# Kernel tuning notes

Hardware: AMD Instinct MI355X
Metric: run time of the kernel (lower is better)

Reference implementation:

```python
import jax, jax.numpy as jnp
import numpy as np

N, E, G = 8192, 65536, 16          # nodes, edges, graphs
EMBED, HID, L = 512, 1024, 3       # embed_dim, hidden_dim, hidden_layers
NG, RBF_R = 50, 12.0               # num_gaussians, rbf_radius
AVG_LEN = 60.0
IN_DIM = 3 * EMBED


def _mlp_params(key, in_dim, hid, out_dim, n_layers):
    ks = jax.random.split(key, 6)
    s_in = 1.0 / np.sqrt(in_dim)
    s_h = 1.0 / np.sqrt(hid)
    return dict(
        in_w=jax.random.normal(ks[0], (in_dim, hid), jnp.float32) * s_in,
        in_b=jnp.zeros((hid,), jnp.float32),
        hid_w=jax.random.normal(ks[1], (n_layers, hid, hid), jnp.float32) * s_h,
        hid_b=jnp.zeros((n_layers, hid), jnp.float32),
        out_w=jax.random.normal(ks[2], (hid, out_dim), jnp.float32) * s_h,
        out_b=jnp.zeros((out_dim,), jnp.float32),
    )


def setup_inputs() -> dict:
    key = jax.random.key(0)
    k = jax.random.split(key, 8)
    x = jax.random.normal(k[0], (N, EMBED), jnp.float32)
    edge_index = jax.random.randint(k[1], (2, E), 0, N, dtype=jnp.int32)
    batch = jnp.sort(jax.random.randint(k[2], (N,), 0, G, dtype=jnp.int32))
    dist = jax.random.uniform(k[3], (E,), jnp.float32) * RBF_R
    v = jax.random.normal(k[4], (E, 3), jnp.float32)
    vec_hat = v / jnp.linalg.norm(v, axis=-1, keepdims=True)
    rbf_w = jax.random.normal(k[5], (NG, EMBED), jnp.float32) * (1.0 / np.sqrt(NG))
    rbf_b = jnp.zeros((EMBED,), jnp.float32)
    e = _mlp_params(k[6], IN_DIM, HID, 1, L)
    f = _mlp_params(k[7], IN_DIM, HID, 1, L)
    return dict(
        x=x, edge_index=edge_index, batch=batch, dist=dist, vec_hat=vec_hat,
        rbf_w=rbf_w, rbf_b=rbf_b,
        e_in_w=e['in_w'], e_in_b=e['in_b'], e_hid_w=e['hid_w'], e_hid_b=e['hid_b'], e_out_w=e['out_w'], e_out_b=e['out_b'],
        f_in_w=f['in_w'], f_in_b=f['in_b'], f_hid_w=f['hid_w'], f_hid_b=f['hid_b'], f_out_w=f['out_w'], f_out_b=f['out_b'],
    )


def _res_mlp(h_in, in_w, in_b, hid_w, hid_b, out_w, out_b):
    h = jax.nn.silu(h_in @ in_w + in_b)           # [E, HID]
    for i in range(L):                             # residual hidden blocks
        h = h + jax.nn.silu(h @ hid_w[i] + hid_b[i])
    return h @ out_w + out_b                       # [E, 1]


def _rbf(dist, rbf_w, rbf_b):
    offsets = jnp.linspace(0.0, RBF_R, NG)
    coeff = -0.5 / (offsets[1] - offsets[0]) ** 2
    g = jnp.exp(coeff * (dist[:, None] - offsets) ** 2)  # [E, NG]
    return g @ rbf_w + rbf_b                              # [E, EMBED]


def reference(x, edge_index, batch, dist, vec_hat,
              rbf_w, rbf_b,
              e_in_w, e_in_b, e_hid_w, e_hid_b, e_out_w, e_out_b,
              f_in_w, f_in_b, f_hid_w, f_hid_b, f_out_w, f_out_b):
    src, dst = edge_index[0], edge_index[1]
    rbf = _rbf(dist, rbf_w, rbf_b)                                 # [E, EMBED]
    inputs = jnp.concatenate([x[src], x[dst], rbf], axis=-1)       # [E, 3*EMBED]
    energy_pairs = _res_mlp(inputs, e_in_w, e_in_b, e_hid_w, e_hid_b, e_out_w, e_out_b)  # [E,1]
    force_pairs = _res_mlp(inputs, f_in_w, f_in_b, f_hid_w, f_hid_b, f_out_w, f_out_b) * vec_hat  # [E,3]
    energy = jax.ops.segment_sum(energy_pairs, batch[src], num_segments=G) / (AVG_LEN ** 2)  # [G,1]
    forces = jax.ops.segment_sum(force_pairs, src, num_segments=N) / AVG_LEN                 # [N,3]
    return energy, forces
```

## Files before the change

kernel.cpp:

```cpp
#include <hip/hip_runtime.h>
#include <math.h>

#define NUM_E 65536
#define NUM_N 8192
#define NUM_G 16
#define RBFR 12.0f

typedef unsigned short u16;
typedef _Float16 f16x8 __attribute__((ext_vector_type(8)));
typedef _Float16 f16x4 __attribute__((ext_vector_type(4)));
typedef float f32x4 __attribute__((ext_vector_type(4)));

#define TILE_F16 8192
#define L1SZ   1114112
#define HSZ    1048576
#define MSTRIDE 4259840

#define FU1  139264
#define FUHL 131072
#define FUPM (FU1 + 3 * FUHL)

#define GLD16(gp, lp) __builtin_amdgcn_global_load_lds( \
    (const __attribute__((address_space(1))) void*)(gp), \
    (__attribute__((address_space(3))) void*)(lp), 16, 0, 0)

#define VMW10() asm volatile("s_waitcnt vmcnt(10)" ::: "memory")
#define VMW8()  asm volatile("s_waitcnt vmcnt(8)" ::: "memory")
#define VMW4()  asm volatile("s_waitcnt vmcnt(4)" ::: "memory")
#define VMW0()  asm volatile("s_waitcnt vmcnt(0)" ::: "memory")
#define BARX()  __builtin_amdgcn_s_barrier()

__global__ void wrbf_kernel(const float* __restrict__ rbf_w, const float* __restrict__ rbf_b,
                            const float* __restrict__ e_in_w, const float* __restrict__ e_in_b,
                            const float* __restrict__ f_in_w, const float* __restrict__ f_in_b,
                            float* __restrict__ wrbf_e, float* __restrict__ b1_e,
                            float* __restrict__ wrbf_f, float* __restrict__ b1_f) {
  int blk = blockIdx.x;
  int mlp = blk / 204;
  int rr = blk % 204;
  int row = rr >> 2;
  int ns = rr & 3;
  const float* in_w = mlp ? f_in_w : e_in_w;
  const float* in_b = mlp ? f_in_b : e_in_b;
  float* wrbf = mlp ? wrbf_f : wrbf_e;
  float* b1   = mlp ? b1_f : b1_e;
  __shared__ float vec[512];
  __shared__ float4 red[256];
  int tid = threadIdx.x;
  vec[tid]       = (row < 50) ? rbf_w[row * 512 + tid]       : rbf_b[tid];
  vec[tid + 256] = (row < 50) ? rbf_w[row * 512 + tid + 256] : rbf_b[tid + 256];
  __syncthreads();
  int q = tid >> 6, l = tid & 63;
  int n0 = ns * 256 + l * 4;
  float a0 = 0.f, a1 = 0.f, a2 = 0.f, a3 = 0.f;
#pragma unroll 4
  for (int c = q * 128; c < q * 128 + 128; ++c) {
    float4 wv = *(const float4*)&in_w[(size_t)(1024 + c) * 1024 + n0];
    float gv = vec[c];
    a0 += gv * wv.x; a1 += gv * wv.y; a2 += gv * wv.z; a3 += gv * wv.w;
  }
  red[tid] = float4{a0, a1, a2, a3};
  __syncthreads();
  if (q == 0) {
    float4 s0 = red[l], s1 = red[l + 64], s2 = red[l + 128], s3 = red[l + 192];
    float4 o = {s0.x + s1.x + s2.x + s3.x, s0.y + s1.y + s2.y + s3.y,
                s0.z + s1.z + s2.z + s3.z, s0.w + s1.w + s2.w + s3.w};
    if (row < 50) {
      *(float4*)&wrbf[row * 1024 + n0] = o;
    } else {
      o.x += in_b[n0]; o.y += in_b[n0 + 1]; o.z += in_b[n0 + 2]; o.w += in_b[n0 + 3];
      *(float4*)&b1[n0] = o;
    }
  }
}

__global__ void prep_kernel(const float* __restrict__ x, const float* __restrict__ dist,
                            u16* __restrict__ xh, u16* __restrict__ grbf) {
  int bid = blockIdx.x, tid = threadIdx.x;
  if (bid < 4096) {
    int i = bid * 256 + tid;
    float4 v = ((const float4*)x)[i];
    f16x4 h = {(_Float16)v.x, (_Float16)v.y, (_Float16)v.z, (_Float16)v.w};
    *(f16x4*)(xh + (size_t)i * 4) = h;
  } else {
    int u = (bid - 4096) * 256 + tid;
    int e = u >> 3, q = u & 7;
    const float delta = RBFR / 49.f;
    const float coeff = -0.5f / (delta * delta);
    float d = dist[e];
    f16x8 h;
#pragma unroll
    for (int j = 0; j < 8; ++j) {
      int gi = q * 8 + j;
      float dd = d - (float)gi * delta;
      float gg = (gi < 50) ? __expf(coeff * dd * dd) : 0.f;
      h[j] = (_Float16)gg;
    }
    *(f16x8*)(grbf + (size_t)u * 8) = h;
  }
}

__global__ void pack_gemm(const float* __restrict__ e_in_w, const float* __restrict__ e_hid_w,
                          const float* __restrict__ f_in_w, const float* __restrict__ f_hid_w,
                          const float* __restrict__ wrbf_e, const float* __restrict__ wrbf_f,
                          u16* __restrict__ wp) {
  __shared__ __align__(16) u16 tile[TILE_F16];
  int bid = blockIdx.x;
  int mlpi = (bid >= 520) ? 1 : 0;
  int t = bid - mlpi * 520;
  const float* in_w  = mlpi ? f_in_w : e_in_w;
  const float* hid_w = mlpi ? f_hid_w : e_hid_w;
  const float* wrbf  = mlpi ? wrbf_f : wrbf_e;
  int tid = threadIdx.x;
  int bnp, nhp, k0, lay = 0, is_l1;
  if (t < 136) {
    int grp = t / 17; int kt = t % 17;
    bnp = grp >> 1; nhp = grp & 1; k0 = kt * 64; is_l1 = 1;
  } else {
    int th = t - 136; lay = th >> 7; int t2 = th & 127;
    bnp = t2 >> 5; nhp = (t2 >> 4) & 1; k0 = (t2 & 15) * 64; is_l1 = 0;
  }
#pragma unroll
  for (int it = 0; it < 8; ++it) {
    int flat = it * 1024 + tid * 4;
    int k = flat >> 7;
    int nl4 = flat & 127;
    int n0 = bnp * 256 + ((nl4 >> 5) << 6) + nhp * 32 + (nl4 & 31);
    int kg = k0 + k;
    float4 v;
    if (is_l1) {
      if (kg < 1024)      v = *(const float4*)&in_w[(size_t)kg * 1024 + n0];
      else if (kg < 1074) v = *(const float4*)&wrbf[(size_t)(kg - 1024) * 1024 + n0];
      else                v = float4{0.f, 0.f, 0.f, 0.f};
    } else {
      v = *(const float4*)&hid_w[(size_t)((lay << 10) + kg) * 1024 + n0];
    }
#pragma unroll
    for (int c = 0; c < 4; ++c) {
      int nl = nl4 + c;
      int pos = nl * 64 + ((((k >> 3) ^ (nl & 7)) << 3) | (k & 7));
      _Float16 hf = (_Float16)(((const float*)&v)[c]);
      tile[pos] = __builtin_bit_cast(u16, hf);
    }
  }
  __syncthreads();
  u16* dst = wp + (size_t)mlpi * MSTRIDE + (size_t)t * TILE_F16;
#pragma unroll
  for (int i = 0; i < 4; ++i) {
    int off = (i * 256 + tid) * 8;
    *(f16x8*)(dst + off) = *(const f16x8*)(tile + off);
  }
}


#define STA(b, ah, kt) do { \
  _Pragma("unroll") for (int _j = 0; _j < 2; ++_j) { \
    int _ck = wv * 2 + _j; \
    int _loc = _ck * 8 + (lane >> 3); \
    int _row = ((_loc >> 6) << 7) + (ah) * 64 + (_loc & 63); \
    int _sw = ((lane & 7) ^ (_loc & 7)) << 3; \
    const u16* _gp; \
    if (MODE == 1) { \
      if ((kt) < 16) { \
        int _nd = ((kt) < 8) ? s_src[_row] : s_dst[_row]; \
        _gp = hin + ((size_t)_nd * 512 + ((kt) & 7) * 64 + _sw); \
      } else { \
        _gp = grbf + ((size_t)(eg0 + _row) * 64 + _sw); \
      } \
    } else { \
      _gp = hin + ((size_t)(rowb + _row) * 1024 + (kt) * 64 + _sw); \
    } \
    GLD16(_gp, (char*)&sm[b][ah][0] + _ck * 1024); \
  } \
} while (0)

#define STB(b, bh, kt) do { \
  const u16* _wt = wl + ((size_t)((bn * 2 + (bh)) * NKT + (kt))) * TILE_F16; \
  _Pragma("unroll") for (int _j = 0; _j < 2; ++_j) { \
    int _ck = wv * 2 + _j; \
    GLD16(_wt + _ck * 512 + lane * 8, (char*)&sm[b][2 + (bh)][0] + _ck * 1024); \
  } \
} while (0)

#define RDA(b, mh) do { \
  _Pragma("unroll") for (int _ks = 0; _ks < 2; ++_ks) { \
    int _kk = _ks * 4 + (lane >> 4); \
    _Pragma("unroll") for (int _m = 0; _m < 4; ++_m) { \
      int _r = wm * 64 + _m * 16 + (lane & 15); \
      af[_m][_ks] = *(const f16x8*)&sm[b][mh][_r * 64 + ((_kk ^ (_r & 7)) << 3)]; \
    } \
  } \
} while (0)

#define RDB(b, nh) do { \
  _Pragma("unroll") for (int _ks = 0; _ks < 2; ++_ks) { \
    int _kk = _ks * 4 + (lane >> 4); \
    _Pragma("unroll") for (int _n = 0; _n < 2; ++_n) { \
      int _c = wn * 32 + _n * 16 + (lane & 15); \
      bf[nh][_n][_ks] = *(const f16x8*)&sm[b][2 + (nh)][_c * 64 + ((_kk ^ (_c & 7)) << 3)]; \
    } \
  } \
} while (0)

#define PHM(mh, nh) do { \
  __builtin_amdgcn_s_setprio(1); \
  _Pragma("unroll") for (int _ks = 0; _ks < 2; ++_ks) \
    _Pragma("unroll") for (int _m = 0; _m < 4; ++_m) \
      _Pragma("unroll") for (int _n = 0; _n < 2; ++_n) \
        acc[(mh) * 4 + _m][(nh) * 2 + _n] = __builtin_amdgcn_mfma_f32_16x16x32_f16( \
            bf[nh][_n][_ks], af[_m][_ks], acc[(mh) * 4 + _m][(nh) * 2 + _n], 0, 0, 0); \
  __builtin_amdgcn_s_setprio(0); \
} while (0)

template<int NKT, int MODE>
__global__ __launch_bounds__(512, 2) void gemm8k(
    const u16* __restrict__ hinE, const u16* __restrict__ hinF,
    const u16* __restrict__ grbf, const int* __restrict__ eidx,
    const int* __restrict__ batch, const float* __restrict__ vhat,
    const u16* __restrict__ wp, size_t woff,
    const float* __restrict__ biasE, const float* __restrict__ biasF,
    u16* __restrict__ houtE, u16* __restrict__ houtF,
    const float* __restrict__ owE, const float* __restrict__ owF,
    const float* __restrict__ obE, const float* __restrict__ obF,
    float* __restrict__ out, int mstart) {
  __shared__ __align__(16) u16 sm[2][4][8192];
  __shared__ int s_src[256];
  __shared__ int s_dst[256];
  __shared__ float sred[256];
  __shared__ float sbins[16];
  const int tid = threadIdx.x;
  const int lane = tid & 63;
  const int wv = tid >> 6;
  const int wm = wv >> 2, wn = wv & 3;

  int mlp, mt, bn;
  {
    int xcd = blockIdx.x & 7;
    int r = blockIdx.x >> 3;
    if (MODE == 1) {
      int bnq = r & 7;
      mlp = bnq >> 2; bn = bnq & 3;
      mt = (r >> 3) * 8 + xcd;
    } else {
      bn = r & 3; mlp = (r >> 2) & 1;
      mt = (r >> 3) * 8 + xcd;
    }
  }
  const u16* hin = (MODE == 1) ? hinE : (mlp ? hinF : hinE);
  const u16* wl = wp + (size_t)mlp * MSTRIDE + woff;
  const float* bias = mlp ? biasF : biasE;
  u16* hout = mlp ? houtF : houtE;
  const int rowb = mt * 256;
  const int n0 = bn * 256;
  const int eg0 = mstart + rowb;

  if (MODE == 1) {
    if (tid < 256) s_src[tid] = eidx[eg0 + tid];
    else s_dst[tid - 256] = eidx[NUM_E + eg0 + tid - 256];
    __syncthreads();
  }

  f32x4 acc[8][4];
#pragma unroll
  for (int m = 0; m < 8; ++m)
#pragma unroll
    for (int n = 0; n < 4; ++n)
#pragma unroll
      for (int i = 0; i < 4; ++i) acc[m][n][i] = 0.f;

  f16x8 af[4][2], bf[2][2][2];

  STA(0, 0, 0); STB(0, 0, 0); STB(0, 1, 0); STA(0, 1, 0);
  VMW4(); BARX();

  for (int t = 0; t < NKT - 1; ++t) {
    const int b = t & 1, nb = b ^ 1;
    STA(nb, 0, t + 1); STB(nb, 0, t + 1); STB(nb, 1, t + 1); STA(nb, 1, t + 1);
    RDA(b, 0); RDB(b, 0);
    VMW10(); BARX();
    PHM(0, 0);
    RDB(b, 1);
    VMW8(); BARX();
    PHM(0, 1);
    RDA(b, 1);
    PHM(1, 0);
    VMW4(); BARX();
    PHM(1, 1);
  }
  {
    const int tb = (NKT - 1) & 1;
    RDA(tb, 0); RDB(tb, 0);
    PHM(0, 0);
    VMW0(); BARX();
    RDB(tb, 1); PHM(0, 1);
    RDA(tb, 1); PHM(1, 0); PHM(1, 1);
  }

  if (MODE != 2) {
#pragma unroll
    for (int mi = 0; mi < 8; ++mi) {
#pragma unroll
      for (int ni = 0; ni < 4; ++ni) {
        int grow = rowb + wm * 128 + mi * 16 + (lane & 15);
        int gn = n0 + wn * 64 + ni * 16 + ((lane >> 4) << 2);
        float4 bi = *(const float4*)&bias[gn];
        f16x4 o;
        if (MODE == 1) {
#pragma unroll
          for (int i = 0; i < 4; ++i) {
            float pre = acc[mi][ni][i] + ((const float*)&bi)[i];
            o[i] = (_Float16)(pre / (1.f + __expf(-pre)));
          }
        } else {
          f16x4 hp = *(const f16x4*)&hin[(size_t)grow * 1024 + gn];
#pragma unroll
          for (int i = 0; i < 4; ++i) {
            float pre = acc[mi][ni][i] + ((const float*)&bi)[i];
            o[i] = (_Float16)(pre / (1.f + __expf(-pre)) + (float)hp[i]);
          }
        }
        *(f16x4*)&hout[(size_t)grow * 1024 + gn] = o;
      }
    }
  } else {
    if (tid < 256) sred[tid] = 0.f;
    if (tid < 16) sbins[tid] = 0.f;
    __syncthreads();
    const float* ow = mlp ? owF : owE;
    float p[8];
#pragma unroll
    for (int mi = 0; mi < 8; ++mi) p[mi] = 0.f;
#pragma unroll
    for (int mi = 0; mi < 8; ++mi) {
#pragma unroll
      for (int ni = 0; ni < 4; ++ni) {
        int grow = rowb + wm * 128 + mi * 16 + (lane & 15);
        int gn = n0 + wn * 64 + ni * 16 + ((lane >> 4) << 2);
        float4 bi = *(const float4*)&bias[gn];
        float4 wv4 = *(const float4*)&ow[gn];
        f16x4 hp = *(const f16x4*)&hin[(size_t)grow * 1024 + gn];
#pragma unroll
        for (int i = 0; i < 4; ++i) {
          float pre = acc[mi][ni][i] + ((const float*)&bi)[i];
          float val = pre / (1.f + __expf(-pre)) + (float)hp[i];
          p[mi] += val * ((const float*)&wv4)[i];
        }
      }
    }
#pragma unroll
    for (int mi = 0; mi < 8; ++mi) {
      p[mi] += __shfl_down(p[mi], 32, 64);
      p[mi] += __shfl_down(p[mi], 16, 64);
    }
    if ((lane >> 4) == 0) {
#pragma unroll
      for (int mi = 0; mi < 8; ++mi)
        atomicAdd(&sred[wm * 128 + mi * 16 + (lane & 15)], p[mi]);
    }
    __syncthreads();
    if (tid < 256) {
      float s = sred[tid];
      int eg = eg0 + tid;
      int si = eidx[eg];
      if (mlp == 0) {
        float pv = s + ((bn == 0) ? obE[0] : 0.f);
        atomicAdd(&sbins[batch[si]], pv);
      } else {
        float pv = (s + ((bn == 0) ? obF[0] : 0.f)) * (1.f / 60.f);
        atomicAdd(&out[16 + si * 3 + 0], pv * vhat[(size_t)eg * 3 + 0]);
        atomicAdd(&out[16 + si * 3 + 1], pv * vhat[(size_t)eg * 3 + 1]);
        atomicAdd(&out[16 + si * 3 + 2], pv * vhat[(size_t)eg * 3 + 2]);
      }
    }
    __syncthreads();
    if (mlp == 0 && tid < 16) atomicAdd(&out[tid], sbins[tid] * (1.f / 3600.f));
  }
}

#define FSWZ(row, col) ((((row) * 1088) + (col)) ^ (((row) & 7) << 3))

__global__ void packF_kernel(const float* __restrict__ e_in_w, const float* __restrict__ e_hid_w,
                             const float* __restrict__ f_in_w, const float* __restrict__ f_hid_w,
                             const float* __restrict__ wrbf_e, const float* __restrict__ wrbf_f,
                             u16* __restrict__ wp) {
  int u = blockIdx.x * 256 + threadIdx.x;
  if (u >= 2 * FUPM) return;
  int m = (u >= FUPM) ? 1 : 0;
  int v = u - m * FUPM;
  const float* in_w  = m ? f_in_w : e_in_w;
  const float* hid_w = m ? f_hid_w : e_hid_w;
  const float* wrbf  = m ? wrbf_f : wrbf_e;
  int l = v & 63;
  int kb = (l >> 4) << 3;
  f16x8 vals;
  if (v < FU1) {
    int kt = v >> 12;
    int ntg = (v >> 6) & 63;
    int n = ntg * 16 + (l & 15);
    int k0 = kt * 32 + kb;
#pragma unroll
    for (int jj = 0; jj < 8; ++jj) {
      int k = k0 + jj;
      float f = (k < 1024) ? in_w[(size_t)k * 1024 + n]
              : ((k < 1074) ? wrbf[(k - 1024) * 1024 + n] : 0.f);
      vals[jj] = (_Float16)f;
    }
  } else {
    int vh = v - FU1;
    int lay = vh >> 17;
    int kt = (vh >> 12) & 31;
    int ntg = (vh >> 6) & 63;
    int n = ntg * 16 + (l & 15);
    int k0 = kt * 32 + kb;
#pragma unroll
    for (int jj = 0; jj < 8; ++jj)
      vals[jj] = (_Float16)hid_w[(size_t)((lay << 10) + k0 + jj) * 1024 + n];
  }
  *(f16x8*)(wp + (size_t)u * 8) = vals;
}

#define F_LOADB(buf, kt) do { \
  const u16* _wr = wl + ((size_t)((kt) * 64 + wave * 8) * 64 + lane) * 8; \
  _Pragma("unroll") \
  for (int _nt = 0; _nt < 8; ++_nt) buf[_nt] = *(const f16x8*)(_wr + (size_t)_nt * 512); \
} while (0)
#define F_LOADA(buf, kt) do { \
  const int _kb = (kt) * 32 + ((lane >> 4) << 3); \
  _Pragma("unroll") \
  for (int _r = 0; _r < 4; ++_r) buf[_r] = *(const f16x8*)&Alds[FSWZ(_r * 16 + (lane & 15), _kb)]; \
} while (0)
#define F_MFMAS(abuf, bbuf) do { \
  _Pragma("unroll") \
  for (int _nt = 0; _nt < 8; ++_nt) \
    _Pragma("unroll") \
    for (int _r = 0; _r < 4; ++_r) \
      acc[_r][_nt] = __builtin_amdgcn_mfma_f32_16x16x32_f16(abuf[_r], bbuf[_nt], acc[_r][_nt], 0, 0, 0); \
} while (0)

__global__ __launch_bounds__(512, 2) void fusedF_kernel(
    const float* __restrict__ x, const int* __restrict__ eidx,
    const int* __restrict__ batch, const float* __restrict__ dist,
    const float* __restrict__ vhat,
    const u16* __restrict__ wp,
    const float* __restrict__ b1_e, const float* __restrict__ b1_f,
    const float* __restrict__ e_hid_b, const float* __restrict__ f_hid_b,
    const float* __restrict__ e_out_w, const float* __restrict__ e_out_b,
    const float* __restrict__ f_out_w, const float* __restrict__ f_out_b,
    float* __restrict__ out) {
  __shared__ __align__(16) u16 Alds[64 * 1088];
  __shared__ float sow[1024];
  __shared__ float sbins[16];
  __shared__ int s_src[64];
  __shared__ int s_dst[64];
  __shared__ float s_dist[64];
  const int tid = threadIdx.x;
  const int lane = tid & 63;
  const int wave = tid >> 6;
  const int e0 = blockIdx.x * 64;
  if (tid < 16) sbins[tid] = 0.f;
  if (tid < 64) s_src[tid] = eidx[e0 + tid];
  if (tid >= 64 && tid < 128) s_dst[tid - 64] = eidx[NUM_E + e0 + tid - 64];
  if (tid >= 128 && tid < 192) s_dist[tid - 128] = dist[e0 + tid - 128];
  __syncthreads();
  const float delta = RBFR / 49.f;
  const float coeff = -0.5f / (delta * delta);
  for (int mlp = 0; mlp < 2; ++mlp) {
    for (int i = tid; i < 16384; i += 512) {
      int e = i >> 8;
      int part = (i >> 7) & 1;
      int q = i & 127;
      int nrow = part ? s_dst[e] : s_src[e];
      float4 v = ((const float4*)x)[(size_t)nrow * 128 + q];
      int col = part * 512 + q * 4;
      f16x4 hv = {(_Float16)v.x, (_Float16)v.y, (_Float16)v.z, (_Float16)v.w};
      *(f16x4*)&Alds[FSWZ(e, col)] = hv;
    }
    for (int i = tid; i < 4096; i += 512) {
      int e = i >> 6;
      int gi = i & 63;
      float d = s_dist[e] - (float)gi * delta;
      float g2 = (gi < 50) ? __expf(coeff * d * d) : 0.f;
      _Float16 hg = (_Float16)g2;
      Alds[FSWZ(e, 1024 + gi)] = __builtin_bit_cast(u16, hg);
    }
    __syncthreads();
    const u16* wp1 = wp + (size_t)mlp * FUPM * 8;
    const u16* wph = wp1 + (size_t)FU1 * 8;
    const float* b1 = mlp ? b1_f : b1_e;
    const float* hb = mlp ? f_hid_b : e_hid_b;
    for (int layer = 0; layer < 4; ++layer) {
      const int nkt = (layer == 0) ? 34 : 32;
      const u16* wl = (layer == 0) ? wp1 : (wph + (size_t)(layer - 1) * FUHL * 8);
      const float* bias = (layer == 0) ? b1 : (hb + (layer - 1) * 1024);
      f32x4 acc[4][8];
#pragma unroll
      for (int r = 0; r < 4; ++r)
#pragma unroll
        for (int nt = 0; nt < 8; ++nt)
#pragma unroll
          for (int i = 0; i < 4; ++i) acc[r][nt][i] = 0.f;
      f16x8 a0[4], a1[4], b0[8], b1r[8];
      F_LOADA(a0, 0); F_LOADB(b0, 0);
      F_LOADA(a1, 1); F_LOADB(b1r, 1);
      for (int kt = 0; kt < nkt; kt += 2) {
        F_MFMAS(a0, b0);
        if (kt + 2 < nkt) { F_LOADA(a0, kt + 2); F_LOADB(b0, kt + 2); }
        F_MFMAS(a1, b1r);
        if (kt + 3 < nkt) { F_LOADA(a1, kt + 3); F_LOADB(b1r, kt + 3); }
      }
      __syncthreads();
      float bia[8];
#pragma unroll
      for (int nt = 0; nt < 8; ++nt) bia[nt] = bias[wave * 128 + nt * 16 + (lane & 15)];
#pragma unroll
      for (int r = 0; r < 4; ++r) {
#pragma unroll
        for (int nt = 0; nt < 8; ++nt) {
#pragma unroll
          for (int i = 0; i < 4; ++i) {
            int row = r * 16 + ((lane >> 4) << 2) + i;
            int col = wave * 128 + nt * 16 + (lane & 15);
            float pre = acc[r][nt][i] + bia[nt];
            float val = pre / (1.f + __expf(-pre));
            int idx = FSWZ(row, col);
            if (layer > 0) {
              _Float16 oldh = __builtin_bit_cast(_Float16, Alds[idx]);
              val += (float)oldh;
            }
            _Float16 nh = (_Float16)val;
            Alds[idx] = __builtin_bit_cast(u16, nh);
          }
        }
      }
      __syncthreads();
    }
    const float* ow = mlp ? f_out_w : e_out_w;
    for (int i = tid; i < 1024; i += 512) sow[i] = ow[i];
    __syncthreads();
    {
      int e = tid >> 3;
      int part = tid & 7;
      float s = 0.f;
#pragma unroll
      for (int cc = 0; cc < 16; ++cc) {
        int col = part * 128 + cc * 8;
        f16x8 hv = *(const f16x8*)&Alds[FSWZ(e, col)];
#pragma unroll
        for (int q = 0; q < 8; ++q) s += (float)hv[q] * sow[col + q];
      }
      s += __shfl_down(s, 4, 8);
      s += __shfl_down(s, 2, 8);
      s += __shfl_down(s, 1, 8);
      if (part == 0) {
        if (mlp == 0) {
          float pp = s + e_out_b[0];
          int gg = batch[s_src[e]];
          atomicAdd(&sbins[gg], pp);
        } else {
          float pp = (s + f_out_b[0]) * (1.f / 60.f);
          int si = s_src[e];
          atomicAdd(&out[16 + si * 3 + 0], pp * vhat[(size_t)(e0 + e) * 3 + 0]);
          atomicAdd(&out[16 + si * 3 + 1], pp * vhat[(size_t)(e0 + e) * 3 + 1]);
          atomicAdd(&out[16 + si * 3 + 2], pp * vhat[(size_t)(e0 + e) * 3 + 2]);
        }
      }
    }
    __syncthreads();
  }
  if (tid < 16) atomicAdd(&out[tid], sbins[tid] * (1.f / 3600.f));
}

extern "C" void kernel_launch(void* const* d_in, const int* in_sizes, int n_in,
                              void* d_out, int out_size, void* d_ws, size_t ws_size,
                              hipStream_t stream) {
  (void)in_sizes; (void)n_in;
  const float* x      = (const float*)d_in[0];
  const int*   eidx   = (const int*)d_in[1];
  const int*   batch  = (const int*)d_in[2];
  const float* dist   = (const float*)d_in[3];
  const float* vhat   = (const float*)d_in[4];
  const float* rbf_w  = (const float*)d_in[5];
  const float* rbf_b  = (const float*)d_in[6];
  const float* e_in_w = (const float*)d_in[7];
  const float* e_in_b = (const float*)d_in[8];
  const float* e_hid_w = (const float*)d_in[9];
  const float* e_hid_b = (const float*)d_in[10];
  const float* e_out_w = (const float*)d_in[11];
  const float* e_out_b = (const float*)d_in[12];
  const float* f_in_w = (const float*)d_in[13];
  const float* f_in_b = (const float*)d_in[14];
  const float* f_hid_w = (const float*)d_in[15];
  const float* f_hid_b = (const float*)d_in[16];
  const float* f_out_w = (const float*)d_in[17];
  const float* f_out_b = (const float*)d_in[18];

  const size_t WP_BYTES = 17039360;
  u16* wp       = (u16*)d_ws;
  float* wrbf_e = (float*)((char*)d_ws + WP_BYTES);
  float* wrbf_f = wrbf_e + 50 * 1024;
  float* b1_e   = wrbf_f + 50 * 1024;
  float* b1_f   = b1_e + 1024;
  const size_t BASE = WP_BYTES + 409600 + 8192;
  u16* xh   = (u16*)((char*)d_ws + BASE);
  u16* grbf = (u16*)((char*)d_ws + BASE + 8388608);
  const size_t FIXED = BASE + 16777216;

  int nch = 0;
  for (int c = 1; c <= 8; c <<= 1) {
    size_t need = FIXED + 4 * (size_t)(NUM_E / c) * 1024 * sizeof(u16);
    if (need <= ws_size) { nch = c; break; }
  }

  hipMemsetAsync(d_out, 0, (size_t)out_size * sizeof(float), stream);
  wrbf_kernel<<<408, 256, 0, stream>>>(rbf_w, rbf_b, e_in_w, e_in_b, f_in_w, f_in_b,
                                       wrbf_e, b1_e, wrbf_f, b1_f);

  if (nch == 0) {
    packF_kernel<<<(2 * FUPM + 255) / 256, 256, 0, stream>>>(
        e_in_w, e_hid_w, f_in_w, f_hid_w, wrbf_e, wrbf_f, wp);
    fusedF_kernel<<<NUM_E / 64, 512, 0, stream>>>(x, eidx, batch, dist, vhat, wp,
                                                  b1_e, b1_f, e_hid_b, f_hid_b,
                                                  e_out_w, e_out_b, f_out_w, f_out_b,
                                                  (float*)d_out);
    return;
  }

  pack_gemm<<<1040, 256, 0, stream>>>(
      e_in_w, e_hid_w, f_in_w, f_hid_w, wrbf_e, wrbf_f, wp);
  prep_kernel<<<6144, 256, 0, stream>>>(x, dist, xh, grbf);

  const int Mchunk = NUM_E / nch;
  u16* hE0 = (u16*)((char*)d_ws + FIXED);
  u16* hE1 = hE0 + (size_t)Mchunk * 1024;
  u16* hF0 = hE1 + (size_t)Mchunk * 1024;
  u16* hF1 = hF0 + (size_t)Mchunk * 1024;
  float* out = (float*)d_out;

  for (int c = 0; c < nch; ++c) {
    int mstart = c * Mchunk;
    int grid = Mchunk / 32;
    gemm8k<17, 1><<<grid, 512, 0, stream>>>(
        xh, xh, grbf, eidx, batch, vhat, wp, 0,
        b1_e, b1_f, hE0, hF0, e_out_w, f_out_w, e_out_b, f_out_b, out, mstart);
    gemm8k<16, 0><<<grid, 512, 0, stream>>>(
        hE0, hF0, grbf, eidx, batch, vhat, wp, L1SZ,
        e_hid_b, f_hid_b, hE1, hF1, e_out_w, f_out_w, e_out_b, f_out_b, out, mstart);
    gemm8k<16, 0><<<grid, 512, 0, stream>>>(
        hE1, hF1, grbf, eidx, batch, vhat, wp, L1SZ + HSZ,
        e_hid_b + 1024, f_hid_b + 1024, hE0, hF0, e_out_w, f_out_w, e_out_b, f_out_b, out, mstart);
    gemm8k<16, 2><<<grid, 512, 0, stream>>>(
        hE0, hF0, grbf, eidx, batch, vhat, wp, L1SZ + 2 * HSZ,
        e_hid_b + 2048, f_hid_b + 2048, hE1, hF1, e_out_w, f_out_w, e_out_b, f_out_b, out, mstart);
  }
}
```

Before: 1.522 ms.

## Switch GEMM inner loop to 32x32x16 MFMA and precompute gather offsets

Replaces the 16x16x32 f16 MFMA tiling with 32x32x16 MFMA instructions. Fragment reads, accumulator layout and epilogue indexing are reorganized to match, which means fewer MFMA issues and fewer LDS fragment reads per tile. It also precomputes the per-thread gather offsets for src, dst and rbf rows once per block, so the global-to-LDS staging no longer re-reads the shared index arrays every k-step. The cost is more live registers per thread, which could hurt occupancy under the 512x2 launch bounds.

```diff
diff --git a/kernel.cpp b/kernel.cpp
--- a/kernel.cpp
+++ b/kernel.cpp
@@ -10,6 +10,7 @@
 typedef _Float16 f16x8 __attribute__((ext_vector_type(8)));
 typedef _Float16 f16x4 __attribute__((ext_vector_type(4)));
 typedef float f32x4 __attribute__((ext_vector_type(4)));
+typedef float f32x16 __attribute__((ext_vector_type(16)));
 
 #define TILE_F16 8192
 #define L1SZ   1114112
@@ -156,18 +157,15 @@
 #define STA(b, ah, kt) do { \
   _Pragma("unroll") for (int _j = 0; _j < 2; ++_j) { \
     int _ck = wv * 2 + _j; \
-    int _loc = _ck * 8 + (lane >> 3); \
-    int _row = ((_loc >> 6) << 7) + (ah) * 64 + (_loc & 63); \
-    int _sw = ((lane & 7) ^ (_loc & 7)) << 3; \
     const u16* _gp; \
     if (MODE == 1) { \
-      if ((kt) < 16) { \
-        int _nd = ((kt) < 8) ? s_src[_row] : s_dst[_row]; \
-        _gp = hin + ((size_t)_nd * 512 + ((kt) & 7) * 64 + _sw); \
-      } else { \
-        _gp = grbf + ((size_t)(eg0 + _row) * 64 + _sw); \
-      } \
+      int _off = ((kt) < 8) ? (osrc[ah][_j] + (kt) * 64) \
+               : (((kt) < 16) ? (odst[ah][_j] + ((kt) - 8) * 64) : ogr[ah][_j]); \
+      _gp = (((kt) < 16) ? hin : grbf) + _off; \
     } else { \
+      int _loc = _ck * 8 + (lane >> 3); \
+      int _row = ((_loc >> 6) << 7) + (ah) * 64 + (_loc & 63); \
+      int _sw = ((lane & 7) ^ (_loc & 7)) << 3; \
       _gp = hin + ((size_t)(rowb + _row) * 1024 + (kt) * 64 + _sw); \
     } \
     GLD16(_gp, (char*)&sm[b][ah][0] + _ck * 1024); \
@@ -182,33 +180,30 @@
   } \
 } while (0)
 
-#define RDA(b, mh) do { \
-  _Pragma("unroll") for (int _ks = 0; _ks < 2; ++_ks) { \
-    int _kk = _ks * 4 + (lane >> 4); \
-    _Pragma("unroll") for (int _m = 0; _m < 4; ++_m) { \
-      int _r = wm * 64 + _m * 16 + (lane & 15); \
-      af[_m][_ks] = *(const f16x8*)&sm[b][mh][_r * 64 + ((_kk ^ (_r & 7)) << 3)]; \
+#define RDA32(b, pair) do { \
+  _Pragma("unroll") for (int _pm = 0; _pm < 2; ++_pm) { \
+    int _r = wm * 64 + _pm * 32 + (lane & 31); \
+    _Pragma("unroll") for (int _sk = 0; _sk < 4; ++_sk) { \
+      int _gk = _sk * 2 + (lane >> 5); \
+      af[_pm][_sk] = *(const f16x8*)&sm[b][pair][_r * 64 + ((_gk ^ (_r & 7)) << 3)]; \
     } \
   } \
 } while (0)
 
-#define RDB(b, nh) do { \
-  _Pragma("unroll") for (int _ks = 0; _ks < 2; ++_ks) { \
-    int _kk = _ks * 4 + (lane >> 4); \
-    _Pragma("unroll") for (int _n = 0; _n < 2; ++_n) { \
-      int _c = wn * 32 + _n * 16 + (lane & 15); \
-      bf[nh][_n][_ks] = *(const f16x8*)&sm[b][2 + (nh)][_c * 64 + ((_kk ^ (_c & 7)) << 3)]; \
-    } \
+#define RDB32(b, ni) do { \
+  int _c = wn * 32 + (lane & 31); \
+  _Pragma("unroll") for (int _sk = 0; _sk < 4; ++_sk) { \
+    int _gk = _sk * 2 + (lane >> 5); \
+    bf[ni][_sk] = *(const f16x8*)&sm[b][2 + (ni)][_c * 64 + ((_gk ^ (_c & 7)) << 3)]; \
   } \
 } while (0)
 
-#define PHM(mh, nh) do { \
+#define PHM32(pair, ni) do { \
   __builtin_amdgcn_s_setprio(1); \
-  _Pragma("unroll") for (int _ks = 0; _ks < 2; ++_ks) \
-    _Pragma("unroll") for (int _m = 0; _m < 4; ++_m) \
-      _Pragma("unroll") for (int _n = 0; _n < 2; ++_n) \
-        acc[(mh) * 4 + _m][(nh) * 2 + _n] = __builtin_amdgcn_mfma_f32_16x16x32_f16( \
-            bf[nh][_n][_ks], af[_m][_ks], acc[(mh) * 4 + _m][(nh) * 2 + _n], 0, 0, 0); \
+  _Pragma("unroll") for (int _sk = 0; _sk < 4; ++_sk) \
+    _Pragma("unroll") for (int _pm = 0; _pm < 2; ++_pm) \
+      acc[(pair) * 2 + _pm][ni] = __builtin_amdgcn_mfma_f32_32x32x16_f16( \
+          bf[ni][_sk], af[_pm][_sk], acc[(pair) * 2 + _pm][ni], 0, 0, 0); \
   __builtin_amdgcn_s_setprio(0); \
 } while (0)
 
@@ -254,21 +249,35 @@
   const int n0 = bn * 256;
   const int eg0 = mstart + rowb;
 
+  int osrc[2][2], odst[2][2], ogr[2][2];
   if (MODE == 1) {
     if (tid < 256) s_src[tid] = eidx[eg0 + tid];
     else s_dst[tid - 256] = eidx[NUM_E + eg0 + tid - 256];
     __syncthreads();
-  }
-
-  f32x4 acc[8][4];
-#pragma unroll
-  for (int m = 0; m < 8; ++m)
-#pragma unroll
-    for (int n = 0; n < 4; ++n)
-#pragma unroll
-      for (int i = 0; i < 4; ++i) acc[m][n][i] = 0.f;
-
-  f16x8 af[4][2], bf[2][2][2];
+#pragma unroll
+    for (int ah = 0; ah < 2; ++ah) {
+#pragma unroll
+      for (int j = 0; j < 2; ++j) {
+        int ck = wv * 2 + j;
+        int loc = ck * 8 + (lane >> 3);
+        int row = ((loc >> 6) << 7) + ah * 64 + (loc & 63);
+        int sw = ((lane & 7) ^ (loc & 7)) << 3;
+        osrc[ah][j] = s_src[row] * 512 + sw;
+        odst[ah][j] = s_dst[row] * 512 + sw;
+        ogr[ah][j]  = (eg0 + row) * 64 + sw;
+      }
+    }
+  }
+
+  f32x16 acc[4][2];
+#pragma unroll
+  for (int m = 0; m < 4; ++m)
+#pragma unroll
+    for (int n = 0; n < 2; ++n)
+#pragma unroll
+      for (int i = 0; i < 16; ++i) acc[m][n][i] = 0.f;
+
+  f16x8 af[2][4], bf[2][4];
 
   STA(0, 0, 0); STB(0, 0, 0); STB(0, 1, 0); STA(0, 1, 0);
   VMW4(); BARX();
@@ -276,50 +285,53 @@
   for (int t = 0; t < NKT - 1; ++t) {
     const int b = t & 1, nb = b ^ 1;
     STA(nb, 0, t + 1); STB(nb, 0, t + 1); STB(nb, 1, t + 1); STA(nb, 1, t + 1);
-    RDA(b, 0); RDB(b, 0);
+    RDA32(b, 0); RDB32(b, 0);
     VMW10(); BARX();
-    PHM(0, 0);
-    RDB(b, 1);
+    PHM32(0, 0);
+    RDB32(b, 1);
     VMW8(); BARX();
-    PHM(0, 1);
-    RDA(b, 1);
-    PHM(1, 0);
+    PHM32(0, 1);
+    RDA32(b, 1);
+    PHM32(1, 0);
     VMW4(); BARX();
-    PHM(1, 1);
+    PHM32(1, 1);
   }
   {
     const int tb = (NKT - 1) & 1;
-    RDA(tb, 0); RDB(tb, 0);
-    PHM(0, 0);
+    RDA32(tb, 0); RDB32(tb, 0);
+    PHM32(0, 0);
     VMW0(); BARX();
-    RDB(tb, 1); PHM(0, 1);
-    RDA(tb, 1); PHM(1, 0); PHM(1, 1);
+    RDB32(tb, 1); PHM32(0, 1);
+    RDA32(tb, 1); PHM32(1, 0); PHM32(1, 1);
   }
 
   if (MODE != 2) {
 #pragma unroll
-    for (int mi = 0; mi < 8; ++mi) {
-#pragma unroll
-      for (int ni = 0; ni < 4; ++ni) {
-        int grow = rowb + wm * 128 + mi * 16 + (lane & 15);
-        int gn = n0 + wn * 64 + ni * 16 + ((lane >> 4) << 2);
-        float4 bi = *(const float4*)&bias[gn];
-        f16x4 o;
-        if (MODE == 1) {
-#pragma unroll
-          for (int i = 0; i < 4; ++i) {
-            float pre = acc[mi][ni][i] + ((const float*)&bi)[i];
-            o[i] = (_Float16)(pre / (1.f + __expf(-pre)));
+    for (int mi = 0; mi < 4; ++mi) {
+      int grow = rowb + wm * 128 + mi * 32 + (lane & 31);
+#pragma unroll
+      for (int ni = 0; ni < 2; ++ni) {
+#pragma unroll
+        for (int q = 0; q < 4; ++q) {
+          int gnb = n0 + wn * 64 + ni * 32 + q * 8 + ((lane >> 5) << 2);
+          float4 bi = *(const float4*)&bias[gnb];
+          f16x4 o;
+          if (MODE == 1) {
+#pragma unroll
+            for (int i = 0; i < 4; ++i) {
+              float pre = acc[mi][ni][q * 4 + i] + ((const float*)&bi)[i];
+              o[i] = (_Float16)(pre / (1.f + __expf(-pre)));
+            }
+          } else {
+            f16x4 hp = *(const f16x4*)&hin[(size_t)grow * 1024 + gnb];
+#pragma unroll
+            for (int i = 0; i < 4; ++i) {
+              float pre = acc[mi][ni][q * 4 + i] + ((const float*)&bi)[i];
+              o[i] = (_Float16)(pre / (1.f + __expf(-pre)) + (float)hp[i]);
+            }
           }
-        } else {
-          f16x4 hp = *(const f16x4*)&hin[(size_t)grow * 1024 + gn];
-#pragma unroll
-          for (int i = 0; i < 4; ++i) {
-            float pre = acc[mi][ni][i] + ((const float*)&bi)[i];
-            o[i] = (_Float16)(pre / (1.f + __expf(-pre)) + (float)hp[i]);
-          }
+          *(f16x4*)&hout[(size_t)grow * 1024 + gnb] = o;
         }
-        *(f16x4*)&hout[(size_t)grow * 1024 + gn] = o;
       }
     }
   } else {
@@ -327,35 +339,35 @@
     if (tid < 16) sbins[tid] = 0.f;
     __syncthreads();
     const float* ow = mlp ? owF : owE;
-    float p[8];
-#pragma unroll
-    for (int mi = 0; mi < 8; ++mi) p[mi] = 0.f;
-#pragma unroll
-    for (int mi = 0; mi < 8; ++mi) {
-#pragma unroll
-      for (int ni = 0; ni < 4; ++ni) {
-        int grow = rowb + wm * 128 + mi * 16 + (lane & 15);
-        int gn = n0 + wn * 64 + ni * 16 + ((lane >> 4) << 2);
-        float4 bi = *(const float4*)&bias[gn];
-        float4 wv4 = *(const float4*)&ow[gn];
-        f16x4 hp = *(const f16x4*)&hin[(size_t)grow * 1024 + gn];
-#pragma unroll
-        for (int i = 0; i < 4; ++i) {
-          float pre = acc[mi][ni][i] + ((const float*)&bi)[i];
-          float val = pre / (1.f + __expf(-pre)) + (float)hp[i];
-          p[mi] += val * ((const float*)&wv4)[i];
+    float p[4];
+#pragma unroll
+    for (int mi = 0; mi < 4; ++mi) p[mi] = 0.f;
+#pragma unroll
+    for (int mi = 0; mi < 4; ++mi) {
+      int grow = rowb + wm * 128 + mi * 32 + (lane & 31);
+#pragma unroll
+      for (int ni = 0; ni < 2; ++ni) {
+#pragma unroll
+        for (int q = 0; q < 4; ++q) {
+          int gnb = n0 + wn * 64 + ni * 32 + q * 8 + ((lane >> 5) << 2);
+          float4 bi = *(const float4*)&bias[gnb];
+          float4 wv4 = *(const float4*)&ow[gnb];
+          f16x4 hp = *(const f16x4*)&hin[(size_t)grow * 1024 + gnb];
+#pragma unroll
+          for (int i = 0; i < 4; ++i) {
+            float pre = acc[mi][ni][q * 4 + i] + ((const float*)&bi)[i];
+            float val = pre / (1.f + __expf(-pre)) + (float)hp[i];
+            p[mi] += val * ((const float*)&wv4)[i];
+          }
         }
       }
     }
 #pragma unroll
-    for (int mi = 0; mi < 8; ++mi) {
-      p[mi] += __shfl_down(p[mi], 32, 64);
-      p[mi] += __shfl_down(p[mi], 16, 64);
-    }
-    if ((lane >> 4) == 0) {
-#pragma unroll
-      for (int mi = 0; mi < 8; ++mi)
-        atomicAdd(&sred[wm * 128 + mi * 16 + (lane & 15)], p[mi]);
+    for (int mi = 0; mi < 4; ++mi) p[mi] += __shfl_down(p[mi], 32, 64);
+    if (lane < 32) {
+#pragma unroll
+      for (int mi = 0; mi < 4; ++mi)
+        atomicAdd(&sred[wm * 128 + mi * 32 + lane], p[mi]);
     }
     __syncthreads();
     if (tid < 256) {
```

New measurement: 1.657 ms. 1.09x slower.
